# Kernel optimization log

Hardware: AMD Instinct MI355X
Metric: run time of the kernel (lower is better)

The kernel has to match this reference:

```python
import jax, jax.numpy as jnp
import numpy as np

N = 100000   # nodes
E = 1600000  # edges (before self-loops)
G = 64       # graphs in batch
IN = 8
H = 4        # heads
EPS_BN = 1e-5

def setup_inputs() -> dict:
    key = jax.random.key(0)
    ks = jax.random.split(key, 30)
    def nrm(k, shape, s=0.1):
        return jax.random.normal(k, shape, dtype=jnp.float32) * s
    inp = {}
    inp['x'] = nrm(ks[0], (N, IN), 1.0)
    inp['edge_index'] = jax.random.randint(ks[1], (2, E), 0, N)
    inp['batch'] = jnp.sort(jax.random.randint(ks[2], (N,), 0, G))
    # GATConv 1: 8 -> 64, 4 heads (concat=False)
    inp['W1'] = nrm(ks[3], (IN, H * 64)); inp['aS1'] = nrm(ks[4], (H, 64)); inp['aD1'] = nrm(ks[5], (H, 64)); inp['b1'] = jnp.zeros((64,), jnp.float32)
    inp['g1'] = jnp.ones((64,), jnp.float32); inp['be1'] = jnp.zeros((64,), jnp.float32)
    # GATConv 2: 64 -> 64
    inp['W2'] = nrm(ks[6], (64, H * 64)); inp['aS2'] = nrm(ks[7], (H, 64)); inp['aD2'] = nrm(ks[8], (H, 64)); inp['b2'] = jnp.zeros((64,), jnp.float32)
    inp['g2'] = jnp.ones((64,), jnp.float32); inp['be2'] = jnp.zeros((64,), jnp.float32)
    # GATConv 3: 64 -> 32
    inp['W3'] = nrm(ks[9], (64, H * 32)); inp['aS3'] = nrm(ks[10], (H, 32)); inp['aD3'] = nrm(ks[11], (H, 32)); inp['b3'] = jnp.zeros((32,), jnp.float32)
    inp['g3'] = jnp.ones((32,), jnp.float32); inp['be3'] = jnp.zeros((32,), jnp.float32)
    # predictor MLP 32 -> 16 -> 1
    inp['Wp1'] = nrm(ks[12], (32, 16)); inp['bp1'] = jnp.zeros((16,), jnp.float32)
    inp['Wp2'] = nrm(ks[13], (16, 1)); inp['bp2'] = jnp.zeros((1,), jnp.float32)
    return inp

def gat_layer(x, src, dst, W, a_src, a_dst, bias, D):
    # x: [N, Fin]; src/dst: [E'] (self-loops included). PyG GATConv semantics.
    h = (x @ W).reshape(N, H, D)                       # [N,H,D]
    alpha_s = jnp.einsum('nhd,hd->nh', h, a_src)       # [N,H]
    alpha_d = jnp.einsum('nhd,hd->nh', h, a_dst)
    e = jax.nn.leaky_relu(alpha_s[src] + alpha_d[dst], 0.2)  # [E',H]
    # segment softmax over incoming edges of each target node
    m = jax.ops.segment_max(e, dst, num_segments=N)
    e = jnp.exp(e - m[dst])
    s = jax.ops.segment_sum(e, dst, num_segments=N)
    alpha = e / (s[dst] + 1e-16)                       # [E',H]
    out = jax.ops.segment_sum(h[src] * alpha[:, :, None], dst, num_segments=N)  # [N,H,D]
    return out.mean(axis=1) + bias                     # concat=False -> head mean

def batch_norm(x, gamma, beta):
    m = x.mean(0)
    v = x.var(0)
    return (x - m) * jax.lax.rsqrt(v + EPS_BN) * gamma + beta

def reference(x, edge_index, batch,
              W1, aS1, aD1, b1, g1, be1,
              W2, aS2, aD2, b2, g2, be2,
              W3, aS3, aD3, b3, g3, be3,
              Wp1, bp1, Wp2, bp2):
    loop = jnp.arange(N)
    src = jnp.concatenate([edge_index[0], loop])  # add self loops (PyG default)
    dst = jnp.concatenate([edge_index[1], loop])
    h = jax.nn.relu(gat_layer(x, src, dst, W1, aS1, aD1, b1, 64))
    h = batch_norm(h, g1, be1)
    h = jax.nn.relu(gat_layer(h, src, dst, W2, aS2, aD2, b2, 64))
    h = batch_norm(h, g2, be2)
    h = jax.nn.relu(gat_layer(h, src, dst, W3, aS3, aD3, b3, 32))
    h = batch_norm(h, g3, be3)
    # global mean pool over graphs
    cnt = jax.ops.segment_sum(jnp.ones((N,), h.dtype), batch, num_segments=G)
    pooled = jax.ops.segment_sum(h, batch, num_segments=G) / jnp.maximum(cnt, 1.0)[:, None]
    hid = jax.nn.relu(pooled @ Wp1 + bp1)
    return hid @ Wp2 + bp2  # [G,1]
```

## Files before the change

### kernel.cpp

```cpp
#include <hip/hip_runtime.h>
#include <hip/hip_fp16.h>

#define N_NODES 100000
#define N_EDGES 1600000
#define EP (N_EDGES + N_NODES)
#define NG 64
#define NH 4
#define POOL_NPB 256
#define BSHIFT 7
#define BNODES 128
#define NBUCK 782
#define BCAP 3072
#define BCHUNK 4096

static inline int cdiv(int a, int b) { return (a + b - 1) / b; }

typedef _Float16 half8 __attribute__((ext_vector_type(8)));
typedef float f32x4 __attribute__((ext_vector_type(4)));

__device__ __forceinline__ float lrelu(float x) { return x >= 0.f ? x : 0.2f * x; }

__global__ __launch_bounds__(256) void k_bucket(const int* __restrict__ ei,
                                                int* __restrict__ gCursor,
                                                unsigned int* __restrict__ pairs) {
  __shared__ int cnt[NBUCK];
  __shared__ int base[NBUCK];
  int tid = threadIdx.x;
  for (int b = tid; b < NBUCK; b += 256) cnt[b] = 0;
  __syncthreads();
  int e0 = blockIdx.x * BCHUNK;
  unsigned int stV[16];
  int stB[16];
#pragma unroll
  for (int i = 0; i < 16; i++) {
    int e = e0 + i * 256 + tid;
    stB[i] = -1;
    if (e < EP) {
      int d, s;
      if (e < N_EDGES) {
        d = __builtin_nontemporal_load(&ei[N_EDGES + e]);
        s = __builtin_nontemporal_load(&ei[e]);
      } else {
        d = s = e - N_EDGES;
      }
      int b = d >> BSHIFT;
      stV[i] = ((unsigned int)s << BSHIFT) | (unsigned int)(d & (BNODES - 1));
      stB[i] = b;
      atomicAdd(&cnt[b], 1);
    }
  }
  __syncthreads();
  for (int b = tid; b < NBUCK; b += 256) {
    base[b] = atomicAdd(&gCursor[b], cnt[b]);
    cnt[b] = 0;
  }
  __syncthreads();
#pragma unroll
  for (int i = 0; i < 16; i++) {
    if (stB[i] >= 0) {
      int r = atomicAdd(&cnt[stB[i]], 1);
      pairs[base[stB[i]] + r] = stV[i];
    }
  }
}

__global__ __launch_bounds__(1024) void k_bscan(const int* __restrict__ gCursor,
                                                int* __restrict__ bstart) {
  __shared__ int sh[1024];
  int t = threadIdx.x;
  int v = (t < NBUCK) ? (gCursor[t] - t * BCAP) : 0;
  sh[t] = v;
  __syncthreads();
  for (int off = 1; off < 1024; off <<= 1) {
    int add = (t >= off) ? sh[t - off] : 0;
    __syncthreads();
    sh[t] += add;
    __syncthreads();
  }
  if (t < NBUCK) {
    bstart[t] = sh[t] - v;
    if (t == NBUCK - 1) bstart[NBUCK] = sh[t];
  }
}

__global__ __launch_bounds__(256) void k_build(const unsigned int* __restrict__ pairs,
                                               const int* __restrict__ bstart,
                                               int* __restrict__ indptr, int* __restrict__ esrc) {
  __shared__ int cnt[BNODES];
  __shared__ int exc[BNODES];
  __shared__ int ptr[BNODES];
  __shared__ int eLds[BCAP];
  int b = blockIdx.x;
  int tid = threadIdx.x;
  int obase = bstart[b];
  int nE = bstart[b + 1] - obase;
  int pbase = b * BCAP;
  if (tid < BNODES) cnt[tid] = 0;
  __syncthreads();
  unsigned int stV[12];
#pragma unroll
  for (int i = 0; i < 12; i++) {
    int idx = i * 256 + tid;
    stV[i] = 0xFFFFFFFFu;
    if (idx < nE) {
      unsigned int v = pairs[pbase + idx];
      stV[i] = v;
      atomicAdd(&cnt[v & (BNODES - 1)], 1);
    }
  }
  __syncthreads();
  if (tid < BNODES) ptr[tid] = cnt[tid];
  __syncthreads();
  for (int off = 1; off < BNODES; off <<= 1) {
    int add = (tid < BNODES && tid >= off) ? ptr[tid - off] : 0;
    __syncthreads();
    if (tid < BNODES) ptr[tid] += add;
    __syncthreads();
  }
  if (tid < BNODES) {
    exc[tid] = ptr[tid] - cnt[tid];
    int n = (b << BSHIFT) + tid;
    if (n < N_NODES) indptr[n] = obase + exc[tid];
    cnt[tid] = 0;
  }
  if (b == NBUCK - 1 && tid == 0) indptr[N_NODES] = bstart[NBUCK];
  __syncthreads();
#pragma unroll
  for (int i = 0; i < 12; i++) {
    if (stV[i] != 0xFFFFFFFFu) {
      int ln = stV[i] & (BNODES - 1);
      int r = atomicAdd(&cnt[ln], 1);
      eLds[exc[ln] + r] = (int)(stV[i] >> BSHIFT);
    }
  }
  __syncthreads();
  for (int idx = tid; idx < nE; idx += 256) esrc[obase + idx] = eLds[idx];
}

template <int FIN, int D>
__device__ void wvec_impl(const float* __restrict__ W, const float* __restrict__ aS,
                          const float* __restrict__ aD, float* __restrict__ wS,
                          float* __restrict__ wD, int t) {
  if (t >= 4 * FIN) return;
  int h = t / FIN, k = t % FIN;
  float ss = 0.f, dd = 0.f;
  for (int d = 0; d < D; d++) {
    float w = W[k * (4 * D) + h * D + d];
    ss = fmaf(w, aS[h * D + d], ss);
    dd = fmaf(w, aD[h * D + d], dd);
  }
  wS[h * FIN + k] = ss;
  wD[h * FIN + k] = dd;
}

template <int D>
__device__ void wcvt_frag(const float* __restrict__ W, __half* __restrict__ wf, int frag, int l) {
  constexpr int NCT = D / 16;
  int kt = frag / NCT, ct = frag % NCT;
  half8 v;
#pragma unroll
  for (int j = 0; j < 8; j++) {
    int kk = kt * 32 + (l >> 4) * 8 + j;
    int k = kk >> 2, h = kk & 3;
    v[j] = (_Float16)W[k * (4 * D) + h * D + ct * 16 + (l & 15)];
  }
  *(half8*)(wf + (size_t)frag * 512 + l * 8) = v;
}

__global__ __launch_bounds__(256) void k_prep(const float* W1, const float* aS1, const float* aD1,
                                              const float* W2, const float* aS2, const float* aD2,
                                              const float* W3, const float* aS3, const float* aD3,
                                              float* wS1, float* wD1, float* wS2, float* wD2,
                                              float* wS3, float* wD3,
                                              __half* wf1, __half* wf2, __half* wf3,
                                              int* gCursor) {
  int b = blockIdx.x, t = threadIdx.x;
  int f = t >> 6, l = t & 63;
  if (b == 0) wvec_impl<8, 64>(W1, aS1, aD1, wS1, wD1, t);
  else if (b == 1) wvec_impl<64, 64>(W2, aS2, aD2, wS2, wD2, t);
  else if (b == 2) wvec_impl<64, 32>(W3, aS3, aD3, wS3, wD3, t);
  else if (b == 3) wcvt_frag<64>(W1, wf1, f, l);
  else if (b < 12) wcvt_frag<64>(W2, wf2, (b - 4) * 4 + f, l);
  else if (b < 16) wcvt_frag<32>(W3, wf3, (b - 12) * 4 + f, l);
  else {
    int idx = (b - 16) * 256 + t;
    if (idx < NBUCK) gCursor[idx] = idx * BCAP;
  }
}

__global__ void k_attdots1(const float* __restrict__ x, const float* __restrict__ wS,
                           const float* __restrict__ wD, float4* __restrict__ as4,
                           float4* __restrict__ ad4) {
  int n = blockIdx.x * blockDim.x + threadIdx.x;
  if (n >= N_NODES) return;
  float4 s = {0, 0, 0, 0}, d = {0, 0, 0, 0};
#pragma unroll
  for (int k = 0; k < 8; k++) {
    float xv = x[(size_t)n * 8 + k];
    s.x = fmaf(xv, wS[k], s.x);
    s.y = fmaf(xv, wS[8 + k], s.y);
    s.z = fmaf(xv, wS[16 + k], s.z);
    s.w = fmaf(xv, wS[24 + k], s.w);
    d.x = fmaf(xv, wD[k], d.x);
    d.y = fmaf(xv, wD[8 + k], d.y);
    d.z = fmaf(xv, wD[16 + k], d.z);
    d.w = fmaf(xv, wD[24 + k], d.w);
  }
  as4[n] = s;
  ad4[n] = d;
}

__global__ __launch_bounds__(256) void k_bnx(const float* __restrict__ tbuf,
                                             const float* __restrict__ scale,
                                             const float* __restrict__ shift,
                                             const float* __restrict__ wS,
                                             const float* __restrict__ wD,
                                             __half* __restrict__ xhat,
                                             float4* __restrict__ as4, float4* __restrict__ ad4) {
  int lane = threadIdx.x & 63;
  int n = blockIdx.x * 4 + (threadIdx.x >> 6);
  if (n >= N_NODES) return;
  float v = fmaf(tbuf[(size_t)n * 64 + lane], scale[lane], shift[lane]);
  xhat[(size_t)n * 64 + lane] = __float2half(v);
  float p0 = v * wS[lane], p1 = v * wS[64 + lane], p2 = v * wS[128 + lane], p3 = v * wS[192 + lane];
  float q0 = v * wD[lane], q1 = v * wD[64 + lane], q2 = v * wD[128 + lane], q3 = v * wD[192 + lane];
#pragma unroll
  for (int off = 32; off; off >>= 1) {
    p0 += __shfl_xor(p0, off); p1 += __shfl_xor(p1, off);
    p2 += __shfl_xor(p2, off); p3 += __shfl_xor(p3, off);
    q0 += __shfl_xor(q0, off); q1 += __shfl_xor(q1, off);
    q2 += __shfl_xor(q2, off); q3 += __shfl_xor(q3, off);
  }
  if (lane == 0) {
    as4[n] = make_float4(p0, p1, p2, p3);
    ad4[n] = make_float4(q0, q1, q2, q3);
  }
}

__global__ __launch_bounds__(256) void k_aggp1(const int* __restrict__ indptr,
                                               const int* __restrict__ esrc,
                                               const float* __restrict__ xg,
                                               const float4* __restrict__ as4,
                                               const float4* __restrict__ ad4,
                                               const __half* __restrict__ wfrag,
                                               const float* __restrict__ bias,
                                               float* __restrict__ tbuf) {
  constexpr int GL = 8, NPW = 8, WB = NPW * (GL + 1);
  __shared__ int sOff[4 * WB];
  __shared__ float4 sW[4 * WB];
  __shared__ __align__(16) __half aT[32 * 40];
  int tid = threadIdx.x;
  int lane = tid & 63;
  int wv = tid >> 6;
  int q = lane & 7;
  int g = lane >> 3;
  int row = wv * 8 + g;
  int n = blockIdx.x * 32 + row;
  int e0 = indptr[n], e1 = indptr[n + 1];
  float4 ad = ad4[n];
  int lbase = wv * WB + g * (GL + 1);
  const char* xb = (const char*)xg + q * 4;
  float s0 = 0.f, s1 = 0.f, s2 = 0.f, s3 = 0.f;
  float a0 = 0.f, a1 = 0.f, a2 = 0.f, a3 = 0.f;
  int c = e0;
  int nc = min(GL, e1 - c);
  int sidx = -1;
  float4 av = make_float4(0.f, 0.f, 0.f, 0.f);
  if (q < nc) { sidx = esrc[c + q]; av = as4[sidx]; }
  while (c < e1) {
    float w0 = 0.f, w1 = 0.f, w2 = 0.f, w3 = 0.f;
    int sB = 0;
    if (sidx >= 0) {
      w0 = __expf(lrelu(av.x + ad.x));
      w1 = __expf(lrelu(av.y + ad.y));
      w2 = __expf(lrelu(av.z + ad.z));
      w3 = __expf(lrelu(av.w + ad.w));
      sB = sidx << 5;
    }
    s0 += w0; s1 += w1; s2 += w2; s3 += w3;
    sOff[lbase + q] = sB;
    sW[lbase + q] = make_float4(w0, w1, w2, w3);
    __builtin_amdgcn_wave_barrier();
    int cn = c + GL;
    int ncn = min(GL, e1 - cn);
    int sidx_n = -1;
    float4 av_n = make_float4(0.f, 0.f, 0.f, 0.f);
    if (cn < e1 && q < ncn) { sidx_n = esrc[cn + q]; av_n = as4[sidx_n]; }
    for (int i = 0; i < nc; ++i) {
      float4 w = sW[lbase + i];
      float xv = *(const float*)(xb + sOff[lbase + i]);
      a0 = fmaf(w.x, xv, a0);
      a1 = fmaf(w.y, xv, a1);
      a2 = fmaf(w.z, xv, a2);
      a3 = fmaf(w.w, xv, a3);
    }
    __builtin_amdgcn_wave_barrier();
    c = cn; nc = ncn; sidx = sidx_n; av = av_n;
  }
#pragma unroll
  for (int off = 1; off < GL; off <<= 1) {
    s0 += __shfl_xor(s0, off);
    s1 += __shfl_xor(s1, off);
    s2 += __shfl_xor(s2, off);
    s3 += __shfl_xor(s3, off);
  }
  float r0 = 1.f / (s0 + 1e-16f), r1 = 1.f / (s1 + 1e-16f);
  float r2 = 1.f / (s2 + 1e-16f), r3 = 1.f / (s3 + 1e-16f);
  __half2 p01 = __floats2half2_rn(a0 * r0, a1 * r1);
  __half2 p23 = __floats2half2_rn(a2 * r2, a3 * r3);
  uint2 pk = make_uint2(*(unsigned*)&p01, *(unsigned*)&p23);
  *(uint2*)&aT[row * 40 + q * 4] = pk;
  __syncthreads();
  int ct = wv;
  int m = lane & 15, kg = lane >> 4;
  half8 bv = *(const half8*)(wfrag + ((size_t)ct * 64 + lane) * 8);
  float bvs = bias[ct * 16 + m];
#pragma unroll
  for (int tt = 0; tt < 2; tt++) {
    half8 avf = *(const half8*)&aT[(tt * 16 + m) * 40 + kg * 8];
    f32x4 cacc = (f32x4){0.f, 0.f, 0.f, 0.f};
    cacc = __builtin_amdgcn_mfma_f32_16x16x32_f16(avf, bv, cacc, 0, 0, 0);
#pragma unroll
    for (int j = 0; j < 4; j++) {
      int nr = blockIdx.x * 32 + tt * 16 + kg * 4 + j;
      tbuf[(size_t)nr * 64 + ct * 16 + m] = fmaxf(fmaf(cacc[j], 0.25f, bvs), 0.f);
    }
  }
}

template <int DOUT>
__global__ __launch_bounds__(256) void k_aggp(const int* __restrict__ indptr,
                                              const int* __restrict__ esrc,
                                              const __half* __restrict__ xg,
                                              const float4* __restrict__ as4,
                                              const float4* __restrict__ ad4,
                                              const __half* __restrict__ wfrag,
                                              const float* __restrict__ bias,
                                              float* __restrict__ tbuf) {
  constexpr int NCT = DOUT / 16;
  constexpr int GL = 16, NPW = 4, WB = NPW * (GL + 1);
  __shared__ int sOff[4 * WB];
  __shared__ float4 sW[4 * WB];
  __shared__ __align__(16) __half aT[16 * 264];
  int tid = threadIdx.x;
  int lane = tid & 63;
  int wv = tid >> 6;
  int q = lane & 15;
  int g = lane >> 4;
  int row = wv * 4 + g;
  int n = blockIdx.x * 16 + row;
  int e0 = indptr[n], e1 = indptr[n + 1];
  float4 ad = ad4[n];
  int lbase = wv * WB + g * (GL + 1);
  const char* xb = (const char*)xg + q * 8;
  float s0 = 0.f, s1 = 0.f, s2 = 0.f, s3 = 0.f;
  float a[4][4];
#pragma unroll
  for (int d = 0; d < 4; d++)
#pragma unroll
    for (int h = 0; h < 4; h++) a[d][h] = 0.f;

  int c = e0;
  int nc = min(GL, e1 - c);
  int sidx = -1;
  float4 av = make_float4(0.f, 0.f, 0.f, 0.f);
  if (q < nc) { sidx = esrc[c + q]; av = as4[sidx]; }
  while (c < e1) {
    float w0 = 0.f, w1 = 0.f, w2 = 0.f, w3 = 0.f;
    int sB = 0;
    if (sidx >= 0) {
      w0 = __expf(lrelu(av.x + ad.x));
      w1 = __expf(lrelu(av.y + ad.y));
      w2 = __expf(lrelu(av.z + ad.z));
      w3 = __expf(lrelu(av.w + ad.w));
      sB = sidx << 7;
    }
    s0 += w0; s1 += w1; s2 += w2; s3 += w3;
    sOff[lbase + q] = sB;
    sW[lbase + q] = make_float4(w0, w1, w2, w3);
    __builtin_amdgcn_wave_barrier();
    int cn = c + GL;
    int ncn = min(GL, e1 - cn);
    int sidx_n = -1;
    float4 av_n = make_float4(0.f, 0.f, 0.f, 0.f);
    if (cn < e1 && q < ncn) { sidx_n = esrc[cn + q]; av_n = as4[sidx_n]; }
    for (int i = 0; i < nc; ++i) {
      float4 w = sW[lbase + i];
      uint2 px = *(const uint2*)(xb + sOff[lbase + i]);
      float2 f01 = __half22float2(*(const __half2*)&px.x);
      float2 f23 = __half22float2(*(const __half2*)&px.y);
      a[0][0] = fmaf(w.x, f01.x, a[0][0]); a[0][1] = fmaf(w.y, f01.x, a[0][1]);
      a[0][2] = fmaf(w.z, f01.x, a[0][2]); a[0][3] = fmaf(w.w, f01.x, a[0][3]);
      a[1][0] = fmaf(w.x, f01.y, a[1][0]); a[1][1] = fmaf(w.y, f01.y, a[1][1]);
      a[1][2] = fmaf(w.z, f01.y, a[1][2]); a[1][3] = fmaf(w.w, f01.y, a[1][3]);
      a[2][0] = fmaf(w.x, f23.x, a[2][0]); a[2][1] = fmaf(w.y, f23.x, a[2][1]);
      a[2][2] = fmaf(w.z, f23.x, a[2][2]); a[2][3] = fmaf(w.w, f23.x, a[2][3]);
      a[3][0] = fmaf(w.x, f23.y, a[3][0]); a[3][1] = fmaf(w.y, f23.y, a[3][1]);
      a[3][2] = fmaf(w.z, f23.y, a[3][2]); a[3][3] = fmaf(w.w, f23.y, a[3][3]);
    }
    __builtin_amdgcn_wave_barrier();
    c = cn; nc = ncn; sidx = sidx_n; av = av_n;
  }
#pragma unroll
  for (int off = 1; off < GL; off <<= 1) {
    s0 += __shfl_xor(s0, off);
    s1 += __shfl_xor(s1, off);
    s2 += __shfl_xor(s2, off);
    s3 += __shfl_xor(s3, off);
  }
  float r0 = 1.f / (s0 + 1e-16f), r1 = 1.f / (s1 + 1e-16f);
  float r2 = 1.f / (s2 + 1e-16f), r3 = 1.f / (s3 + 1e-16f);
  __half2 p[8];
#pragma unroll
  for (int d = 0; d < 4; d++) {
    p[2 * d] = __floats2half2_rn(a[d][0] * r0, a[d][1] * r1);
    p[2 * d + 1] = __floats2half2_rn(a[d][2] * r2, a[d][3] * r3);
  }
  uint4 lo = make_uint4(*(unsigned*)&p[0], *(unsigned*)&p[1], *(unsigned*)&p[2], *(unsigned*)&p[3]);
  uint4 hi = make_uint4(*(unsigned*)&p[4], *(unsigned*)&p[5], *(unsigned*)&p[6], *(unsigned*)&p[7]);
  *(uint4*)&aT[row * 264 + q * 16] = lo;
  *(uint4*)&aT[row * 264 + q * 16 + 8] = hi;
  __syncthreads();
  if (wv < NCT) {
    int ct = wv;
    int m = lane & 15, kg = lane >> 4;
    f32x4 cacc = (f32x4){0.f, 0.f, 0.f, 0.f};
#pragma unroll
    for (int kt = 0; kt < 8; kt++) {
      half8 avf = *(const half8*)&aT[m * 264 + kt * 32 + kg * 8];
      half8 bvf = *(const half8*)(wfrag + ((kt * NCT + ct) * 64 + lane) * 8);
      cacc = __builtin_amdgcn_mfma_f32_16x16x32_f16(avf, bvf, cacc, 0, 0, 0);
    }
    float bv = bias[ct * 16 + m];
#pragma unroll
    for (int j = 0; j < 4; j++) {
      int nr = blockIdx.x * 16 + kg * 4 + j;
      tbuf[(size_t)nr * DOUT + ct * 16 + m] = fmaxf(fmaf(cacc[j], 0.25f, bv), 0.f);
    }
  }
}

template <int C>
__global__ __launch_bounds__(256) void k_bnstat(const float* __restrict__ x, float* __restrict__ part) {
  const int RG = 256 / C;
  int col = threadIdx.x & (C - 1);
  int rg = threadIdx.x / C;
  int rows = (N_NODES + gridDim.x - 1) / gridDim.x;
  int r0 = blockIdx.x * rows;
  int r1 = min(N_NODES, r0 + rows);
  float s = 0.f, q = 0.f;
  for (int r = r0 + rg; r < r1; r += RG) {
    float v = x[(size_t)r * C + col];
    s += v;
    q = fmaf(v, v, q);
  }
  __shared__ float sh[512];
  sh[threadIdx.x] = s;
  sh[256 + threadIdx.x] = q;
  __syncthreads();
  for (int step = 128; step >= C; step >>= 1) {
    if (threadIdx.x < step) {
      sh[threadIdx.x] += sh[threadIdx.x + step];
      sh[256 + threadIdx.x] += sh[256 + threadIdx.x + step];
    }
    __syncthreads();
  }
  if (threadIdx.x < C) {
    part[blockIdx.x * 2 * C + threadIdx.x] = sh[threadIdx.x];
    part[blockIdx.x * 2 * C + C + threadIdx.x] = sh[256 + threadIdx.x];
  }
}

template <int C>
__global__ void k_bnfinal(const float* __restrict__ part, const float* __restrict__ g,
                          const float* __restrict__ be, float* __restrict__ scale,
                          float* __restrict__ shift) {
  int c = threadIdx.x;
  if (c >= C) return;
  float s = 0.f, q = 0.f;
  for (int b = 0; b < 256; b++) {
    s += part[b * 2 * C + c];
    q += part[b * 2 * C + C + c];
  }
  float mean = s / (float)N_NODES;
  float var = q / (float)N_NODES - mean * mean;
  float sc = g[c] * rsqrtf(var + 1e-5f);
  scale[c] = sc;
  shift[c] = be[c] - mean * sc;
}

__global__ __launch_bounds__(256) void k_pool(const float* __restrict__ f3,
                                              const int* __restrict__ batch,
                                              const float* __restrict__ scale,
                                              const float* __restrict__ shift,
                                              float* __restrict__ pool,
                                              float* __restrict__ cntg) {
  __shared__ float acc[NG][33];
  int t = threadIdx.x;
  for (int i = t; i < NG * 33; i += 256) ((float*)acc)[i] = 0.f;
  __syncthreads();
  int c = t & 31, rg = t >> 5;
  float sc = scale[c], sh = shift[c];
  int n0 = blockIdx.x * POOL_NPB;
  int n1 = min(N_NODES, n0 + POOL_NPB);
  float r = 0.f, rc = 0.f;
  int gcur = -1;
  for (int n = n0 + rg; n < n1; n += 8) {
    int g = batch[n];
    if (g != gcur) {
      if (gcur >= 0) {
        atomicAdd(&acc[gcur][c], r);
        if (c == 0) atomicAdd(&acc[gcur][32], rc);
      }
      gcur = g;
      r = 0.f;
      rc = 0.f;
    }
    r += fmaf(f3[(size_t)n * 32 + c], sc, sh);
    rc += 1.f;
  }
  if (gcur >= 0) {
    atomicAdd(&acc[gcur][c], r);
    if (c == 0) atomicAdd(&acc[gcur][32], rc);
  }
  __syncthreads();
  for (int i = t; i < NG * 32; i += 256) {
    int g = i >> 5, cc = i & 31;
    float v = acc[g][cc];
    if (v != 0.f) atomicAdd(&pool[i], v);
  }
  for (int g = t; g < NG; g += 256) {
    float v = acc[g][32];
    if (v != 0.f) atomicAdd(&cntg[g], v);
  }
}

__global__ void k_mlp(const float* __restrict__ pool, const float* __restrict__ cntg,
                      const float* __restrict__ Wp1, const float* __restrict__ bp1,
                      const float* __restrict__ Wp2, const float* __restrict__ bp2,
                      float* __restrict__ out) {
  int g = threadIdx.x;
  if (g >= NG) return;
  float inv = 1.f / fmaxf(cntg[g], 1.f);
  float p[32];
#pragma unroll
  for (int c = 0; c < 32; c++) p[c] = pool[g * 32 + c] * inv;
  float o = bp2[0];
  for (int j = 0; j < 16; j++) {
    float hsum = bp1[j];
#pragma unroll
    for (int c = 0; c < 32; c++) hsum = fmaf(p[c], Wp1[c * 16 + j], hsum);
    o = fmaf(fmaxf(hsum, 0.f), Wp2[j], o);
  }
  out[g] = o;
}

extern "C" void kernel_launch(void* const* d_in, const int* in_sizes, int n_in,
                              void* d_out, int out_size, void* d_ws, size_t ws_size,
                              hipStream_t stream) {
  const float* x = (const float*)d_in[0];
  const int* ei = (const int*)d_in[1];
  const int* batch = (const int*)d_in[2];
  const float* W1 = (const float*)d_in[3];
  const float* aS1 = (const float*)d_in[4];
  const float* aD1 = (const float*)d_in[5];
  const float* b1 = (const float*)d_in[6];
  const float* g1 = (const float*)d_in[7];
  const float* be1 = (const float*)d_in[8];
  const float* W2 = (const float*)d_in[9];
  const float* aS2 = (const float*)d_in[10];
  const float* aD2 = (const float*)d_in[11];
  const float* b2 = (const float*)d_in[12];
  const float* g2 = (const float*)d_in[13];
  const float* be2 = (const float*)d_in[14];
  const float* W3 = (const float*)d_in[15];
  const float* aS3 = (const float*)d_in[16];
  const float* aD3 = (const float*)d_in[17];
  const float* b3 = (const float*)d_in[18];
  const float* g3 = (const float*)d_in[19];
  const float* be3 = (const float*)d_in[20];
  const float* Wp1 = (const float*)d_in[21];
  const float* bp1 = (const float*)d_in[22];
  const float* Wp2 = (const float*)d_in[23];
  const float* bp2 = (const float*)d_in[24];
  float* out = (float*)d_out;

  size_t off = 0;
  auto alloc = [&](size_t bytes) -> void* {
    void* p = (char*)d_ws + off;
    off += (bytes + 255) & ~(size_t)255;
    return p;
  };
  float* pool = (float*)alloc((size_t)NG * 32 * 4);
  float* cntg = (float*)alloc((size_t)NG * 4);
  size_t zbytes = off;
  int* gCursor = (int*)alloc((size_t)NBUCK * 4);
  int* bstart = (int*)alloc((size_t)(NBUCK + 1) * 4);
  unsigned int* pairs = (unsigned int*)alloc((size_t)NBUCK * BCAP * 4);
  int* indptr = (int*)alloc((size_t)(N_NODES + 1) * 4);
  int* esrc = (int*)alloc((size_t)EP * 4);
  __half* xhat = (__half*)alloc((size_t)N_NODES * 64 * 2);
  float* as_ = (float*)alloc((size_t)N_NODES * 16);
  float* ad_ = (float*)alloc((size_t)N_NODES * 16);
  float* tbuf = (float*)alloc((size_t)N_NODES * 64 * 4);
  float* part = (float*)alloc((size_t)256 * 128 * 4);
  float* scale = (float*)alloc(64 * 4);
  float* shift = (float*)alloc(64 * 4);
  float* wS1 = (float*)alloc(32 * 4);
  float* wD1 = (float*)alloc(32 * 4);
  float* wS2 = (float*)alloc(256 * 4);
  float* wD2 = (float*)alloc(256 * 4);
  float* wS3 = (float*)alloc(256 * 4);
  float* wD3 = (float*)alloc(256 * 4);
  __half* wf1 = (__half*)alloc((size_t)4 * 512 * 2);
  __half* wf2 = (__half*)alloc((size_t)32 * 512 * 2);
  __half* wf3 = (__half*)alloc((size_t)16 * 512 * 2);
  if (off > ws_size) return;

  hipMemsetAsync(pool, 0, zbytes, stream);

  k_prep<<<16 + cdiv(NBUCK, 256), 256, 0, stream>>>(W1, aS1, aD1, W2, aS2, aD2, W3, aS3, aD3,
                                                    wS1, wD1, wS2, wD2, wS3, wD3, wf1, wf2, wf3,
                                                    gCursor);
  k_bucket<<<cdiv(EP, BCHUNK), 256, 0, stream>>>(ei, gCursor, pairs);
  k_bscan<<<1, 1024, 0, stream>>>(gCursor, bstart);
  k_build<<<NBUCK, 256, 0, stream>>>(pairs, bstart, indptr, esrc);

  k_attdots1<<<cdiv(N_NODES, 256), 256, 0, stream>>>(x, wS1, wD1, (float4*)as_, (float4*)ad_);
  k_aggp1<<<N_NODES / 32, 256, 0, stream>>>(indptr, esrc, x, (const float4*)as_,
                                            (const float4*)ad_, wf1, b1, tbuf);
  k_bnstat<64><<<256, 256, 0, stream>>>(tbuf, part);
  k_bnfinal<64><<<1, 64, 0, stream>>>(part, g1, be1, scale, shift);

  k_bnx<<<cdiv(N_NODES, 4), 256, 0, stream>>>(tbuf, scale, shift, wS2, wD2, xhat,
                                              (float4*)as_, (float4*)ad_);
  k_aggp<64><<<N_NODES / 16, 256, 0, stream>>>(indptr, esrc, xhat, (const float4*)as_,
                                               (const float4*)ad_, wf2, b2, tbuf);
  k_bnstat<64><<<256, 256, 0, stream>>>(tbuf, part);
  k_bnfinal<64><<<1, 64, 0, stream>>>(part, g2, be2, scale, shift);

  k_bnx<<<cdiv(N_NODES, 4), 256, 0, stream>>>(tbuf, scale, shift, wS3, wD3, xhat,
                                              (float4*)as_, (float4*)ad_);
  k_aggp<32><<<N_NODES / 16, 256, 0, stream>>>(indptr, esrc, xhat, (const float4*)as_,
                                               (const float4*)ad_, wf3, b3, tbuf);
  k_bnstat<32><<<256, 256, 0, stream>>>(tbuf, part);
  k_bnfinal<32><<<1, 32, 0, stream>>>(part, g3, be3, scale, shift);

  k_pool<<<cdiv(N_NODES, POOL_NPB), 256, 0, stream>>>(tbuf, batch, scale, shift, pool, cntg);
  k_mlp<<<1, 64, 0, stream>>>(pool, cntg, Wp1, bp1, Wp2, bp2, out);
}
```

Before: 442.7 us.

## Fuse batch-norm statistics into aggregation epilogues and drop edge prefetch

Each aggregation kernel now accumulates per-column sum and sum-of-squares of its output tile in its epilogue and writes per-block partials. A new per-channel finalize kernel reduces those partials, replacing the separate stats pass that re-read the full feature buffer. This saves one full read of the activations per layer and one launch, at the cost of a larger partials array and a longer final reduction. The software prefetch of the next edge chunk's source indices and attention values is also removed, which simplifies the loop and may lower register pressure but exposes gather latency.

```diff
diff --git a/kernel.cpp b/kernel.cpp
--- a/kernel.cpp
+++ b/kernel.cpp
@@ -12,6 +12,8 @@
 #define NBUCK 782
 #define BCAP 3072
 #define BCHUNK 4096
+#define NBLK2 (N_NODES / 16)
+#define NBLK1 (N_NODES / 32)
 
 static inline int cdiv(int a, int b) { return (a + b - 1) / b; }
 
@@ -244,7 +246,8 @@
                                                const float4* __restrict__ ad4,
                                                const __half* __restrict__ wfrag,
                                                const float* __restrict__ bias,
-                                               float* __restrict__ tbuf) {
+                                               float* __restrict__ tbuf,
+                                               float* __restrict__ part) {
   constexpr int GL = 8, NPW = 8, WB = NPW * (GL + 1);
   __shared__ int sOff[4 * WB];
   __shared__ float4 sW[4 * WB];
@@ -262,15 +265,13 @@
   const char* xb = (const char*)xg + q * 4;
   float s0 = 0.f, s1 = 0.f, s2 = 0.f, s3 = 0.f;
   float a0 = 0.f, a1 = 0.f, a2 = 0.f, a3 = 0.f;
-  int c = e0;
-  int nc = min(GL, e1 - c);
-  int sidx = -1;
-  float4 av = make_float4(0.f, 0.f, 0.f, 0.f);
-  if (q < nc) { sidx = esrc[c + q]; av = as4[sidx]; }
-  while (c < e1) {
+  for (int c = e0; c < e1; c += GL) {
+    int nc = min(GL, e1 - c);
     float w0 = 0.f, w1 = 0.f, w2 = 0.f, w3 = 0.f;
     int sB = 0;
-    if (sidx >= 0) {
+    if (q < nc) {
+      int sidx = esrc[c + q];
+      float4 av = as4[sidx];
       w0 = __expf(lrelu(av.x + ad.x));
       w1 = __expf(lrelu(av.y + ad.y));
       w2 = __expf(lrelu(av.z + ad.z));
@@ -281,11 +282,6 @@
     sOff[lbase + q] = sB;
     sW[lbase + q] = make_float4(w0, w1, w2, w3);
     __builtin_amdgcn_wave_barrier();
-    int cn = c + GL;
-    int ncn = min(GL, e1 - cn);
-    int sidx_n = -1;
-    float4 av_n = make_float4(0.f, 0.f, 0.f, 0.f);
-    if (cn < e1 && q < ncn) { sidx_n = esrc[cn + q]; av_n = as4[sidx_n]; }
     for (int i = 0; i < nc; ++i) {
       float4 w = sW[lbase + i];
       float xv = *(const float*)(xb + sOff[lbase + i]);
@@ -295,7 +291,6 @@
       a3 = fmaf(w.w, xv, a3);
     }
     __builtin_amdgcn_wave_barrier();
-    c = cn; nc = ncn; sidx = sidx_n; av = av_n;
   }
 #pragma unroll
   for (int off = 1; off < GL; off <<= 1) {
@@ -315,6 +310,7 @@
   int m = lane & 15, kg = lane >> 4;
   half8 bv = *(const half8*)(wfrag + ((size_t)ct * 64 + lane) * 8);
   float bvs = bias[ct * 16 + m];
+  float psum = 0.f, psq = 0.f;
 #pragma unroll
   for (int tt = 0; tt < 2; tt++) {
     half8 avf = *(const half8*)&aT[(tt * 16 + m) * 40 + kg * 8];
@@ -323,8 +319,17 @@
 #pragma unroll
     for (int j = 0; j < 4; j++) {
       int nr = blockIdx.x * 32 + tt * 16 + kg * 4 + j;
-      tbuf[(size_t)nr * 64 + ct * 16 + m] = fmaxf(fmaf(cacc[j], 0.25f, bvs), 0.f);
-    }
+      float ov = fmaxf(fmaf(cacc[j], 0.25f, bvs), 0.f);
+      tbuf[(size_t)nr * 64 + ct * 16 + m] = ov;
+      psum += ov;
+      psq = fmaf(ov, ov, psq);
+    }
+  }
+  psum += __shfl_xor(psum, 16); psum += __shfl_xor(psum, 32);
+  psq += __shfl_xor(psq, 16); psq += __shfl_xor(psq, 32);
+  if (kg == 0) {
+    part[(size_t)blockIdx.x * 128 + ct * 16 + m] = psum;
+    part[(size_t)blockIdx.x * 128 + 64 + ct * 16 + m] = psq;
   }
 }
 
@@ -336,7 +341,8 @@
                                               const float4* __restrict__ ad4,
                                               const __half* __restrict__ wfrag,
                                               const float* __restrict__ bias,
-                                              float* __restrict__ tbuf) {
+                                              float* __restrict__ tbuf,
+                                              float* __restrict__ part) {
   constexpr int NCT = DOUT / 16;
   constexpr int GL = 16, NPW = 4, WB = NPW * (GL + 1);
   __shared__ int sOff[4 * WB];
@@ -360,15 +366,13 @@
 #pragma unroll
     for (int h = 0; h < 4; h++) a[d][h] = 0.f;
 
-  int c = e0;
-  int nc = min(GL, e1 - c);
-  int sidx = -1;
-  float4 av = make_float4(0.f, 0.f, 0.f, 0.f);
-  if (q < nc) { sidx = esrc[c + q]; av = as4[sidx]; }
-  while (c < e1) {
+  for (int c = e0; c < e1; c += GL) {
+    int nc = min(GL, e1 - c);
     float w0 = 0.f, w1 = 0.f, w2 = 0.f, w3 = 0.f;
     int sB = 0;
-    if (sidx >= 0) {
+    if (q < nc) {
+      int sidx = esrc[c + q];
+      float4 av = as4[sidx];
       w0 = __expf(lrelu(av.x + ad.x));
       w1 = __expf(lrelu(av.y + ad.y));
       w2 = __expf(lrelu(av.z + ad.z));
@@ -379,11 +383,6 @@
     sOff[lbase + q] = sB;
     sW[lbase + q] = make_float4(w0, w1, w2, w3);
     __builtin_amdgcn_wave_barrier();
-    int cn = c + GL;
-    int ncn = min(GL, e1 - cn);
-    int sidx_n = -1;
-    float4 av_n = make_float4(0.f, 0.f, 0.f, 0.f);
-    if (cn < e1 && q < ncn) { sidx_n = esrc[cn + q]; av_n = as4[sidx_n]; }
     for (int i = 0; i < nc; ++i) {
       float4 w = sW[lbase + i];
       uint2 px = *(const uint2*)(xb + sOff[lbase + i]);
@@ -399,7 +398,6 @@
       a[3][2] = fmaf(w.z, f23.y, a[3][2]); a[3][3] = fmaf(w.w, f23.y, a[3][3]);
     }
     __builtin_amdgcn_wave_barrier();
-    c = cn; nc = ncn; sidx = sidx_n; av = av_n;
   }
 #pragma unroll
   for (int off = 1; off < GL; off <<= 1) {
@@ -432,61 +430,55 @@
       cacc = __builtin_amdgcn_mfma_f32_16x16x32_f16(avf, bvf, cacc, 0, 0, 0);
     }
     float bv = bias[ct * 16 + m];
+    float psum = 0.f, psq = 0.f;
 #pragma unroll
     for (int j = 0; j < 4; j++) {
       int nr = blockIdx.x * 16 + kg * 4 + j;
-      tbuf[(size_t)nr * DOUT + ct * 16 + m] = fmaxf(fmaf(cacc[j], 0.25f, bv), 0.f);
+      float ov = fmaxf(fmaf(cacc[j], 0.25f, bv), 0.f);
+      tbuf[(size_t)nr * DOUT + ct * 16 + m] = ov;
+      psum += ov;
+      psq = fmaf(ov, ov, psq);
+    }
+    psum += __shfl_xor(psum, 16); psum += __shfl_xor(psum, 32);
+    psq += __shfl_xor(psq, 16); psq += __shfl_xor(psq, 32);
+    if (kg == 0) {
+      part[(size_t)blockIdx.x * (2 * DOUT) + ct * 16 + m] = psum;
+      part[(size_t)blockIdx.x * (2 * DOUT) + DOUT + ct * 16 + m] = psq;
     }
   }
 }
 
 template <int C>
-__global__ __launch_bounds__(256) void k_bnstat(const float* __restrict__ x, float* __restrict__ part) {
-  const int RG = 256 / C;
-  int col = threadIdx.x & (C - 1);
-  int rg = threadIdx.x / C;
-  int rows = (N_NODES + gridDim.x - 1) / gridDim.x;
-  int r0 = blockIdx.x * rows;
-  int r1 = min(N_NODES, r0 + rows);
+__global__ __launch_bounds__(256) void k_bnfin2(const float* __restrict__ part, int nb,
+                                                const float* __restrict__ g,
+                                                const float* __restrict__ be,
+                                                float* __restrict__ scale,
+                                                float* __restrict__ shift) {
+  int c = blockIdx.x;
+  int t = threadIdx.x;
   float s = 0.f, q = 0.f;
-  for (int r = r0 + rg; r < r1; r += RG) {
-    float v = x[(size_t)r * C + col];
-    s += v;
-    q = fmaf(v, v, q);
+  for (int b = t; b < nb; b += 256) {
+    s += part[(size_t)b * (2 * C) + c];
+    q += part[(size_t)b * (2 * C) + C + c];
   }
   __shared__ float sh[512];
-  sh[threadIdx.x] = s;
-  sh[256 + threadIdx.x] = q;
-  __syncthreads();
-  for (int step = 128; step >= C; step >>= 1) {
-    if (threadIdx.x < step) {
-      sh[threadIdx.x] += sh[threadIdx.x + step];
-      sh[256 + threadIdx.x] += sh[256 + threadIdx.x + step];
+  sh[t] = s;
+  sh[256 + t] = q;
+  __syncthreads();
+  for (int step = 128; step; step >>= 1) {
+    if (t < step) {
+      sh[t] += sh[t + step];
+      sh[256 + t] += sh[256 + t + step];
     }
     __syncthreads();
   }
-  if (threadIdx.x < C) {
-    part[blockIdx.x * 2 * C + threadIdx.x] = sh[threadIdx.x];
-    part[blockIdx.x * 2 * C + C + threadIdx.x] = sh[256 + threadIdx.x];
-  }
-}
-
-template <int C>
-__global__ void k_bnfinal(const float* __restrict__ part, const float* __restrict__ g,
-                          const float* __restrict__ be, float* __restrict__ scale,
-                          float* __restrict__ shift) {
-  int c = threadIdx.x;
-  if (c >= C) return;
-  float s = 0.f, q = 0.f;
-  for (int b = 0; b < 256; b++) {
-    s += part[b * 2 * C + c];
-    q += part[b * 2 * C + C + c];
-  }
-  float mean = s / (float)N_NODES;
-  float var = q / (float)N_NODES - mean * mean;
-  float sc = g[c] * rsqrtf(var + 1e-5f);
-  scale[c] = sc;
-  shift[c] = be[c] - mean * sc;
+  if (t == 0) {
+    float mean = sh[0] / (float)N_NODES;
+    float var = sh[256] / (float)N_NODES - mean * mean;
+    float sc = g[c] * rsqrtf(var + 1e-5f);
+    scale[c] = sc;
+    shift[c] = be[c] - mean * sc;
+  }
 }
 
 __global__ __launch_bounds__(256) void k_pool(const float* __restrict__ f3,
@@ -603,7 +595,7 @@
   float* as_ = (float*)alloc((size_t)N_NODES * 16);
   float* ad_ = (float*)alloc((size_t)N_NODES * 16);
   float* tbuf = (float*)alloc((size_t)N_NODES * 64 * 4);
-  float* part = (float*)alloc((size_t)256 * 128 * 4);
+  float* part = (float*)alloc((size_t)NBLK2 * 128 * 4);
   float* scale = (float*)alloc(64 * 4);
   float* shift = (float*)alloc(64 * 4);
   float* wS1 = (float*)alloc(32 * 4);
@@ -627,24 +619,21 @@
   k_build<<<NBUCK, 256, 0, stream>>>(pairs, bstart, indptr, esrc);
 
   k_attdots1<<<cdiv(N_NODES, 256), 256, 0, stream>>>(x, wS1, wD1, (float4*)as_, (float4*)ad_);
-  k_aggp1<<<N_NODES / 32, 256, 0, stream>>>(indptr, esrc, x, (const float4*)as_,
-                                            (const float4*)ad_, wf1, b1, tbuf);
-  k_bnstat<64><<<256, 256, 0, stream>>>(tbuf, part);
-  k_bnfinal<64><<<1, 64, 0, stream>>>(part, g1, be1, scale, shift);
+  k_aggp1<<<NBLK1, 256, 0, stream>>>(indptr, esrc, x, (const float4*)as_,
+                                     (const float4*)ad_, wf1, b1, tbuf, part);
+  k_bnfin2<64><<<64, 256, 0, stream>>>(part, NBLK1, g1, be1, scale, shift);
 
   k_bnx<<<cdiv(N_NODES, 4), 256, 0, stream>>>(tbuf, scale, shift, wS2, wD2, xhat,
                                               (float4*)as_, (float4*)ad_);
-  k_aggp<64><<<N_NODES / 16, 256, 0, stream>>>(indptr, esrc, xhat, (const float4*)as_,
-                                               (const float4*)ad_, wf2, b2, tbuf);
-  k_bnstat<64><<<256, 256, 0, stream>>>(tbuf, part);
-  k_bnfinal<64><<<1, 64, 0, stream>>>(part, g2, be2, scale, shift);
+  k_aggp<64><<<NBLK2, 256, 0, stream>>>(indptr, esrc, xhat, (const float4*)as_,
+                                        (const float4*)ad_, wf2, b2, tbuf, part);
+  k_bnfin2<64><<<64, 256, 0, stream>>>(part, NBLK2, g2, be2, scale, shift);
 
   k_bnx<<<cdiv(N_NODES, 4), 256, 0, stream>>>(tbuf, scale, shift, wS3, wD3, xhat,
                                               (float4*)as_, (float4*)ad_);
-  k_aggp<32><<<N_NODES / 16, 256, 0, stream>>>(indptr, esrc, xhat, (const float4*)as_,
-                                               (const float4*)ad_, wf3, b3, tbuf);
-  k_bnstat<32><<<256, 256, 0, stream>>>(tbuf, part);
-  k_bnfinal<32><<<1, 32, 0, stream>>>(part, g3, be3, scale, shift);
+  k_aggp<32><<<NBLK2, 256, 0, stream>>>(indptr, esrc, xhat, (const float4*)as_,
+                                        (const float4*)ad_, wf3, b3, tbuf, part);
+  k_bnfin2<32><<<32, 256, 0, stream>>>(part, NBLK2, g3, be3, scale, shift);
 
   k_pool<<<cdiv(N_NODES, POOL_NPB), 256, 0, stream>>>(tbuf, batch, scale, shift, pool, cntg);
   k_mlp<<<1, 64, 0, stream>>>(pool, cntg, Wp1, bp1, Wp2, bp2, out);
```

After: 382.4 us. 1.16x faster.
